# Kernel optimization log

Hardware: AMD Instinct MI355X
Metric: run time of the kernel (lower is better)

The kernel has to match this reference:

```python
import jax, jax.numpy as jnp
import numpy as np
import math

B_ = 32      # input capsule types
C_ = 32      # output capsule types
K = 3        # kernel
STRIDE = 2
H = 4
HH = H * H
ITER = 3
EPS = 1e-10
LN_2PI = math.log(2.0 * math.pi)


def setup_inputs() -> dict:
    key = jax.random.key(0)
    k1, k2, k3, k4, k5 = jax.random.split(key, 5)
    b, win = 8, 14
    poses = jax.random.normal(k1, (b, B_, win, win, HH), jnp.float32)
    activations = jax.random.uniform(k2, (b, B_, win, win), jnp.float32)
    W = jax.random.normal(k3, (B_, K, K, C_, H, H), jnp.float32)
    beta_v = jax.random.normal(k4, (1, C_, 1, 1), jnp.float32)
    beta_a = jax.random.normal(k5, (1, C_, 1), jnp.float32)
    lambda_ = jnp.float32(0.01)
    return {"poses": poses, "activations": activations, "W": W,
            "beta_v": beta_v, "beta_a": beta_a, "lambda_": lambda_}


def _extract_patches(x, w):
    r = STRIDE * jnp.arange(w)[:, None] + jnp.arange(K)  # [w, K]
    x = x[:, :, r]
    x = x[:, :, :, :, r]        # index width   -> [b,B,w_i,Kr,w_j,Kc,...]
    return x


def _em_routing(lambda_, a_, V, beta_v, beta_a):
    # a_: [b,Bkk,Cww], V: [b,Bkk,Cww,hh]
    b, Bkk, Cww, hh = V.shape
    R = jnp.full((b, Bkk, Cww), 1.0 / C_, V.dtype)
    a = None
    mu = None
    for i in range(ITER):
        Rw = (R * a_)[..., None]                      # [b,Bkk,Cww,1]
        sum_R = Rw.sum(1)                             # [b,Cww,1]
        mu = ((Rw * V).sum(1) / sum_R)[:, None]       # [b,1,Cww,hh]
        V_minus_mu_sqr = (V - mu) ** 2                # [b,Bkk,Cww,hh]
        sigma_sq = ((Rw * V_minus_mu_sqr).sum(1) / sum_R)[:, None]  # [b,1,Cww,hh]
        log_sigma = jnp.log(jnp.sqrt(sigma_sq) + EPS)
        cost = (beta_v + log_sigma.reshape(b, C_, -1, hh)) * sum_R.reshape(b, C_, -1, 1)
        a = jax.nn.sigmoid(lambda_ * (beta_a - cost.sum(-1)))
        a = a.reshape(b, Cww)
        if i != ITER - 1:
            ln_p = -V_minus_mu_sqr / (2.0 * sigma_sq) - log_sigma - 0.5 * LN_2PI
            p = jnp.exp(ln_p)
            ap = a[:, None, :] * p.sum(-1)            # [b,Bkk,Cww]
            R = jax.lax.stop_gradient(ap / (ap.sum(2, keepdims=True) + EPS) + EPS)
    return a, mu


def reference(poses, activations, W, beta_v, beta_a, lambda_):
    b = poses.shape[0]
    win = poses.shape[2]
    w = (win - K) // STRIDE + 1
    Bkk = K * K * B_
    Cww = w * w * C_

    # pose patches, ordered exactly like torch: stacked over (j outer, i inner)
    pp = _extract_patches(poses, w)                 # [b,B,w_i,Kr,w_j,Kc,hh]
    pp = pp.transpose(0, 1, 3, 5, 4, 2, 6)          # [b,B,Kr,Kc,w_j,w_i,hh]
    pp = pp.reshape(b, B_, K, K, w, w, H, H)

    # votes: W[B,Kr,Kc,C,p,q] @ pose[...,q,r]
    votes = jnp.einsum('Buvcpq,bBuvxyqr->bBuvcxypr', W, pp)
    votes = votes.reshape(b, Bkk, Cww, HH)

    # activation patches, repeated over C to match Cww=(C,w,w) flatten order
    ap = _extract_patches(activations, w)           # [b,B,w_i,Kr,w_j,Kc]
    ap = ap.transpose(0, 1, 3, 5, 4, 2).reshape(b, Bkk, w * w)
    a_ = jnp.broadcast_to(ap[:, :, None, :], (b, Bkk, C_, w * w)).reshape(b, Bkk, Cww)

    a, mu = _em_routing(lambda_, a_, votes, beta_v, beta_a)
    return mu.reshape(b, C_, w, w, HH), a.reshape(b, C_, w, w)
```

## Files before the change

### kernel.cpp

```cpp
#include <hip/hip_runtime.h>
#include <math.h>

#define NB   8
#define BC   32
#define WIN  14
#define HH   16
#define BKK  288
#define CWW  1152
#define NXY  36
#define EPSF 1e-10f
#define LOG2E 1.4426950408889634f
#define LN2   0.6931471805599453f
#define L2SQ2PI 1.3257480647361593f

__device__ __forceinline__ float ex2(float x) { return __builtin_amdgcn_exp2f(x); }
__device__ __forceinline__ float lg2(float x) { return __builtin_amdgcn_logf(x); }
__device__ __forceinline__ float rcpf(float x) { return __builtin_amdgcn_rcpf(x); }

__device__ __forceinline__ float red16(float v) {
    v += __shfl_xor(v, 1);
    v += __shfl_xor(v, 2);
    v += __shfl_xor(v, 4);
    v += __shfl_xor(v, 8);
    return v;
}

__device__ __forceinline__ float4 f4mul(float s, float4 b) {
    return make_float4(s * b.x, s * b.y, s * b.z, s * b.w);
}
__device__ __forceinline__ float4 f4fma(float s, float4 b, float4 c) {
    return make_float4(fmaf(s, b.x, c.x), fmaf(s, b.y, c.y),
                       fmaf(s, b.z, c.z), fmaf(s, b.w, c.w));
}

__global__ __launch_bounds__(256)
void wt_kernel(const float4* __restrict__ W4, float4* __restrict__ Wt4) {
    int o = blockIdx.x * 256 + threadIdx.x;
    if (o < BKK * 128) {
        int c = o & 31, p = (o >> 5) & 3, m = o >> 7;
        Wt4[o] = W4[(m * 32 + c) * 4 + p];
    }
}

__global__ __launch_bounds__(256)
void rowred_kernel(const float* __restrict__ rows_part, float* __restrict__ invRowG) {
    int i = blockIdx.x * 256 + threadIdx.x;
    if (i < NB * BKK) {
        int b = i / BKK, m = i % BKK;
        float s = EPSF;
        #pragma unroll 8
        for (int j = 0; j < 72; ++j) s += rows_part[(b * 72 + j) * BKK + m];
        invRowG[i] = 1.0f / s;
    }
}

template<int STAGE, bool FINAL>
__global__ __launch_bounds__(256)
void stats_kernel(const float* __restrict__ poses,
                  const float* __restrict__ act,
                  const float4* __restrict__ Wt4,
                  const float* __restrict__ beta_v,
                  const float* __restrict__ beta_a,
                  const float* __restrict__ lam,
                  const float* __restrict__ aws_in,
                  const float* __restrict__ psum,
                  const float* __restrict__ invRowG,
                  float* __restrict__ mu_out,
                  float* __restrict__ K2n_out,
                  float* __restrict__ C2n_out,
                  float* __restrict__ a_out)
{
    __shared__ float4 poseS4[BKK * 4];
    __shared__ float2 AE[BKK];
    __shared__ float4 red4[4 * 16 * 9];

    const int bid   = blockIdx.x;
    const int chalf = bid & 1;
    const int xy    = (bid >> 1) % NXY;
    const int b     = bid / 72;
    const int X = xy / 6, Y = xy % 6;

    const int tid = threadIdx.x;
    const int c_l = tid & 15;
    const int mch = tid >> 4;
    const int c   = chalf * 16 + c_l;
    const int n   = c * NXY + xy;

    const float4* poses4 = reinterpret_cast<const float4*>(poses);
    for (int idx = tid; idx < BKK * 4; idx += 256) {
        int m = idx >> 2, q = idx & 3;
        int B = m / 9, uv = m % 9, u = uv / 3, v = uv % 3;
        poseS4[idx] = poses4[((b * BC + B) * 196 + (2 * Y + u) * WIN + (2 * X + v)) * 4 + q];
    }
    for (int m = tid; m < BKK; m += 256) {
        int B = m / 9, uv = m % 9, u = uv / 3, v = uv % 3;
        float am = act[(b * BC + B) * 196 + (2 * Y + u) * WIN + (2 * X + v)];
        float ai, ea;
        if constexpr (STAGE == 0) { ai = am * (1.0f / 32.0f); ea = 0.0f; }
        else { ai = am * invRowG[b * BKK + m]; ea = EPSF * am; }
        AE[m] = make_float2(ai, ea);
    }

    float ap_n = 0.0f;
    const float* psum_b = nullptr;
    if constexpr (STAGE >= 1) {
        ap_n   = aws_in[(b * NXY + xy) * 32 + c];
        psum_b = psum + ((b * BKK) * NXY + xy) * 32 + c;
    }
    __syncthreads();

    const float4* WtB = Wt4 + c;

    float  sum_R = 0.0f;
    float4 sRV[4]  = {make_float4(0,0,0,0), make_float4(0,0,0,0), make_float4(0,0,0,0), make_float4(0,0,0,0)};
    float4 sRV2[4] = {make_float4(0,0,0,0), make_float4(0,0,0,0), make_float4(0,0,0,0), make_float4(0,0,0,0)};

    const int m0 = mch * 18;
    #pragma unroll 3
    for (int i = 0; i < 18; ++i) {
        int m = m0 + i;
        float4 w0 = WtB[m * 128 +  0];
        float4 w1 = WtB[m * 128 + 32];
        float4 w2 = WtB[m * 128 + 64];
        float4 w3 = WtB[m * 128 + 96];
        float4 P0 = poseS4[m * 4 + 0];
        float4 P1 = poseS4[m * 4 + 1];
        float4 P2 = poseS4[m * 4 + 2];
        float4 P3 = poseS4[m * 4 + 3];
        float4 V0 = f4fma(w0.w, P3, f4fma(w0.z, P2, f4fma(w0.y, P1, f4mul(w0.x, P0))));
        float4 V1 = f4fma(w1.w, P3, f4fma(w1.z, P2, f4fma(w1.y, P1, f4mul(w1.x, P0))));
        float4 V2 = f4fma(w2.w, P3, f4fma(w2.z, P2, f4fma(w2.y, P1, f4mul(w2.x, P0))));
        float4 V3 = f4fma(w3.w, P3, f4fma(w3.z, P2, f4fma(w3.y, P1, f4mul(w3.x, P0))));
        float Ra;
        if constexpr (STAGE == 0) {
            Ra = AE[m].x;
        } else {
            float ps = psum_b[m * (NXY * 32)];
            float2 ae = AE[m];
            Ra = fmaf(ap_n * ps, ae.x, ae.y);
        }
        sum_R += Ra;
        sRV[0] = f4fma(Ra, V0, sRV[0]);
        sRV[1] = f4fma(Ra, V1, sRV[1]);
        sRV[2] = f4fma(Ra, V2, sRV[2]);
        sRV[3] = f4fma(Ra, V3, sRV[3]);
        float4 q0 = make_float4(V0.x*V0.x, V0.y*V0.y, V0.z*V0.z, V0.w*V0.w);
        float4 q1 = make_float4(V1.x*V1.x, V1.y*V1.y, V1.z*V1.z, V1.w*V1.w);
        float4 q2 = make_float4(V2.x*V2.x, V2.y*V2.y, V2.z*V2.z, V2.w*V2.w);
        float4 q3 = make_float4(V3.x*V3.x, V3.y*V3.y, V3.z*V3.z, V3.w*V3.w);
        sRV2[0] = f4fma(Ra, q0, sRV2[0]);
        sRV2[1] = f4fma(Ra, q1, sRV2[1]);
        sRV2[2] = f4fma(Ra, q2, sRV2[2]);
        sRV2[3] = f4fma(Ra, q3, sRV2[3]);
    }

    {
        float* f1 = reinterpret_cast<float*>(sRV);
        float* f2 = reinterpret_cast<float*>(sRV2);
        #pragma unroll
        for (int k = 0; k < 16; ++k) { f1[k] += __shfl_xor(f1[k], 16); f2[k] += __shfl_xor(f2[k], 16); }
        sum_R += __shfl_xor(sum_R, 16);
        #pragma unroll
        for (int k = 0; k < 16; ++k) { f1[k] += __shfl_xor(f1[k], 32); f2[k] += __shfl_xor(f2[k], 32); }
        sum_R += __shfl_xor(sum_R, 32);
    }
    const int wgrp = tid >> 6;
    if ((tid & 48) == 0) {
        float4* dst = &red4[(wgrp * 16 + c_l) * 9];
        dst[0] = make_float4(sum_R, 0.f, 0.f, 0.f);
        dst[1] = sRV[0];  dst[2] = sRV[1];  dst[3] = sRV[2];  dst[4] = sRV[3];
        dst[5] = sRV2[0]; dst[6] = sRV2[1]; dst[7] = sRV2[2]; dst[8] = sRV2[3];
    }
    __syncthreads();

    const int h  = tid & 15;
    const int cc = tid >> 4;
    const float* red = reinterpret_cast<const float*>(red4);
    float sR = 0.f, sV = 0.f, sV2 = 0.f;
    #pragma unroll
    for (int j = 0; j < 4; ++j) {
        int off = (j * 16 + cc) * 36;
        sR  += red[off];
        sV  += red[off + 4 + h];
        sV2 += red[off + 20 + h];
    }
    float inv = 1.0f / sR;
    float mu  = sV * inv;
    float sig = fmaxf(fmaf(-mu, mu, sV2 * inv), 1e-30f);
    float l2s = lg2(sqrtf(sig) + EPSF);
    float lsum = red16(l2s) * LN2;
    int   cg   = chalf * 16 + cc;
    float cost = sR * fmaf(16.0f, beta_v[cg], lsum);
    float z    = lam[0] * (beta_a[cg] - cost);
    float av   = rcpf(1.0f + ex2(-z * LOG2E));

    int nn   = cg * NXY + xy;
    int base = (b * CWW + nn) * HH + h;
    mu_out[base] = mu;
    if constexpr (!FINAL) {
        K2n_out[base] = (-0.5f * LOG2E) / sig;
        C2n_out[base] = -(l2s + L2SQ2PI);
        if (h == 0) a_out[(b * NXY + xy) * 32 + cg] = av;
    } else {
        if (h == 0) a_out[b * CWW + nn] = av;
    }
}

__global__ __launch_bounds__(256)
void pv_kernel(const float* __restrict__ poses,
               const float4* __restrict__ Wt4,
               const float4* __restrict__ mu4,
               const float4* __restrict__ K4,
               const float4* __restrict__ C4,
               const float* __restrict__ aws,
               float* __restrict__ psum_out,
               float* __restrict__ rows_part)
{
    __shared__ float4 poseS4[BKK * 4];

    const int bid   = blockIdx.x;
    const int chalf = bid & 1;
    const int xy    = (bid >> 1) % NXY;
    const int b     = bid / 72;
    const int X = xy / 6, Y = xy % 6;

    const int tid = threadIdx.x;
    const int c_l = tid & 15;
    const int mch = tid >> 4;
    const int c   = chalf * 16 + c_l;
    const int n   = c * NXY + xy;

    const float4* poses4 = reinterpret_cast<const float4*>(poses);
    for (int idx = tid; idx < BKK * 4; idx += 256) {
        int m = idx >> 2, q = idx & 3;
        int B = m / 9, uv = m % 9, u = uv / 3, v = uv % 3;
        poseS4[idx] = poses4[((b * BC + B) * 196 + (2 * Y + u) * WIN + (2 * X + v)) * 4 + q];
    }

    float4 M[4], Kk[4], Cc[4];
    {
        int nb4 = (b * CWW + n) * 4;
        #pragma unroll
        for (int p = 0; p < 4; ++p) { M[p] = mu4[nb4 + p]; Kk[p] = K4[nb4 + p]; Cc[p] = C4[nb4 + p]; }
    }
    const float ap = aws[(b * NXY + xy) * 32 + c];
    __syncthreads();

    const float4* WtB = Wt4 + c;
    float* ps_out = psum_out + ((b * BKK) * NXY + xy) * 32 + c;
    const int rbase = bid * BKK;

    const int m0 = mch * 18;
    #pragma unroll 3
    for (int i = 0; i < 18; ++i) {
        int m = m0 + i;
        float4 w0 = WtB[m * 128 +  0];
        float4 w1 = WtB[m * 128 + 32];
        float4 w2 = WtB[m * 128 + 64];
        float4 w3 = WtB[m * 128 + 96];
        float4 P0 = poseS4[m * 4 + 0];
        float4 P1 = poseS4[m * 4 + 1];
        float4 P2 = poseS4[m * 4 + 2];
        float4 P3 = poseS4[m * 4 + 3];
        float4 V0 = f4fma(w0.w, P3, f4fma(w0.z, P2, f4fma(w0.y, P1, f4mul(w0.x, P0))));
        float4 V1 = f4fma(w1.w, P3, f4fma(w1.z, P2, f4fma(w1.y, P1, f4mul(w1.x, P0))));
        float4 V2 = f4fma(w2.w, P3, f4fma(w2.z, P2, f4fma(w2.y, P1, f4mul(w2.x, P0))));
        float4 V3 = f4fma(w3.w, P3, f4fma(w3.z, P2, f4fma(w3.y, P1, f4mul(w3.x, P0))));

        float psv = 0.0f;
        {
            float4 t, g;
            t = make_float4(V0.x-M[0].x, V0.y-M[0].y, V0.z-M[0].z, V0.w-M[0].w);
            g = make_float4(fmaf(t.x*t.x, Kk[0].x, Cc[0].x), fmaf(t.y*t.y, Kk[0].y, Cc[0].y),
                            fmaf(t.z*t.z, Kk[0].z, Cc[0].z), fmaf(t.w*t.w, Kk[0].w, Cc[0].w));
            psv += ex2(g.x) + ex2(g.y) + ex2(g.z) + ex2(g.w);
            t = make_float4(V1.x-M[1].x, V1.y-M[1].y, V1.z-M[1].z, V1.w-M[1].w);
            g = make_float4(fmaf(t.x*t.x, Kk[1].x, Cc[1].x), fmaf(t.y*t.y, Kk[1].y, Cc[1].y),
                            fmaf(t.z*t.z, Kk[1].z, Cc[1].z), fmaf(t.w*t.w, Kk[1].w, Cc[1].w));
            psv += ex2(g.x) + ex2(g.y) + ex2(g.z) + ex2(g.w);
            t = make_float4(V2.x-M[2].x, V2.y-M[2].y, V2.z-M[2].z, V2.w-M[2].w);
            g = make_float4(fmaf(t.x*t.x, Kk[2].x, Cc[2].x), fmaf(t.y*t.y, Kk[2].y, Cc[2].y),
                            fmaf(t.z*t.z, Kk[2].z, Cc[2].z), fmaf(t.w*t.w, Kk[2].w, Cc[2].w));
            psv += ex2(g.x) + ex2(g.y) + ex2(g.z) + ex2(g.w);
            t = make_float4(V3.x-M[3].x, V3.y-M[3].y, V3.z-M[3].z, V3.w-M[3].w);
            g = make_float4(fmaf(t.x*t.x, Kk[3].x, Cc[3].x), fmaf(t.y*t.y, Kk[3].y, Cc[3].y),
                            fmaf(t.z*t.z, Kk[3].z, Cc[3].z), fmaf(t.w*t.w, Kk[3].w, Cc[3].w));
            psv += ex2(g.x) + ex2(g.y) + ex2(g.z) + ex2(g.w);
        }
        ps_out[m * (NXY * 32)] = psv;

        float rv = ap * psv;
        rv += __shfl_xor(rv, 1);
        rv += __shfl_xor(rv, 2);
        rv += __shfl_xor(rv, 4);
        rv += __shfl_xor(rv, 8);
        if (c_l == 0) rows_part[rbase + m] = rv;
    }
}

extern "C" void kernel_launch(void* const* d_in, const int* in_sizes, int n_in,
                              void* d_out, int out_size, void* d_ws, size_t ws_size,
                              hipStream_t stream) {
    const float* poses  = (const float*)d_in[0];
    const float* act    = (const float*)d_in[1];
    const float* W      = (const float*)d_in[2];
    const float* beta_v = (const float*)d_in[3];
    const float* beta_a = (const float*)d_in[4];
    const float* lam    = (const float*)d_in[5];
    float* out = (float*)d_out;
    float* ws  = (float*)d_ws;

    const int SZ = NB * CWW * HH;
    float* Wt   = ws;
    float* mu   = Wt + SZ;
    float* K2n  = mu + SZ;
    float* C2n  = K2n + SZ;
    float* aws  = C2n + SZ;
    float* rows = aws + NB * CWW;
    float* invR = rows + NB * 72 * BKK;
    float* psum = invR + NB * BKK;

    const float4* Wt4 = (const float4*)Wt;

    wt_kernel<<<dim3(144), dim3(256), 0, stream>>>((const float4*)W, (float4*)Wt);

    stats_kernel<0, false><<<dim3(576), dim3(256), 0, stream>>>(
        poses, act, Wt4, beta_v, beta_a, lam, nullptr, nullptr, nullptr,
        mu, K2n, C2n, aws);
    pv_kernel<<<dim3(576), dim3(256), 0, stream>>>(
        poses, Wt4, (const float4*)mu, (const float4*)K2n, (const float4*)C2n,
        aws, psum, rows);
    rowred_kernel<<<dim3(9), dim3(256), 0, stream>>>(rows, invR);
    stats_kernel<1, false><<<dim3(576), dim3(256), 0, stream>>>(
        poses, act, Wt4, beta_v, beta_a, lam, aws, psum, invR,
        mu, K2n, C2n, aws);
    pv_kernel<<<dim3(576), dim3(256), 0, stream>>>(
        poses, Wt4, (const float4*)mu, (const float4*)K2n, (const float4*)C2n,
        aws, psum, rows);
    rowred_kernel<<<dim3(9), dim3(256), 0, stream>>>(rows, invR);
    stats_kernel<1, true><<<dim3(576), dim3(256), 0, stream>>>(
        poses, act, Wt4, beta_v, beta_a, lam, aws, psum, invR,
        out, nullptr, nullptr, out + SZ);
}
```

Measured before the change: 180.2 us.

## Fuse routing iterations into one persistent kernel with grid barriers

Replaces the chain of stats, pv and row-reduction kernels with a single persistent kernel of 576 blocks. Each block keeps its pose patch, per-row probabilities, mu/K/C and activations in shared memory across iterations, so those intermediates no longer go through global memory. Grid-wide atomic barriers stand in for the kernel boundaries at the row-sum dependency. This removes several launches and most global traffic, but it depends on all 576 blocks being co-resident (launch bounds request 3 per CU) and adds spin-wait barrier cost.

```diff
diff --git a/kernel.cpp b/kernel.cpp
--- a/kernel.cpp
+++ b/kernel.cpp
@@ -8,6 +8,7 @@
 #define BKK  288
 #define CWW  1152
 #define NXY  36
+#define NBLK 576
 #define EPSF 1e-10f
 #define LOG2E 1.4426950408889634f
 #define LN2   0.6931471805599453f
@@ -42,74 +43,27 @@
     }
 }
 
-__global__ __launch_bounds__(256)
-void rowred_kernel(const float* __restrict__ rows_part, float* __restrict__ invRowG) {
-    int i = blockIdx.x * 256 + threadIdx.x;
-    if (i < NB * BKK) {
-        int b = i / BKK, m = i % BKK;
-        float s = EPSF;
-        #pragma unroll 8
-        for (int j = 0; j < 72; ++j) s += rows_part[(b * 72 + j) * BKK + m];
-        invRowG[i] = 1.0f / s;
-    }
+__device__ __forceinline__ void gridbar(unsigned* bar, unsigned target) {
+    __syncthreads();
+    if (threadIdx.x == 0) {
+        __threadfence();
+        atomicAdd(bar, 1u);
+        while (atomicAdd(bar, 0u) < target) __builtin_amdgcn_s_sleep(2);
+        __threadfence();
+    }
+    __syncthreads();
 }
 
 template<int STAGE, bool FINAL>
-__global__ __launch_bounds__(256)
-void stats_kernel(const float* __restrict__ poses,
-                  const float* __restrict__ act,
-                  const float4* __restrict__ Wt4,
-                  const float* __restrict__ beta_v,
-                  const float* __restrict__ beta_a,
-                  const float* __restrict__ lam,
-                  const float* __restrict__ aws_in,
-                  const float* __restrict__ psum,
-                  const float* __restrict__ invRowG,
-                  float* __restrict__ mu_out,
-                  float* __restrict__ K2n_out,
-                  float* __restrict__ C2n_out,
-                  float* __restrict__ a_out)
+__device__ __forceinline__ void stats_phase(
+    const float4* __restrict__ WtB, const float4* poseS4, const float* psumS,
+    const float* actS, const float* AIS, float* red, float* mKC, float* aS,
+    const float* __restrict__ beta_v, const float* __restrict__ beta_a,
+    float lamv, int tid, int c_l, int mch, int chalf, int xy, int b,
+    float* __restrict__ out)
 {
-    __shared__ float4 poseS4[BKK * 4];
-    __shared__ float2 AE[BKK];
-    __shared__ float4 red4[4 * 16 * 9];
-
-    const int bid   = blockIdx.x;
-    const int chalf = bid & 1;
-    const int xy    = (bid >> 1) % NXY;
-    const int b     = bid / 72;
-    const int X = xy / 6, Y = xy % 6;
-
-    const int tid = threadIdx.x;
-    const int c_l = tid & 15;
-    const int mch = tid >> 4;
-    const int c   = chalf * 16 + c_l;
-    const int n   = c * NXY + xy;
-
-    const float4* poses4 = reinterpret_cast<const float4*>(poses);
-    for (int idx = tid; idx < BKK * 4; idx += 256) {
-        int m = idx >> 2, q = idx & 3;
-        int B = m / 9, uv = m % 9, u = uv / 3, v = uv % 3;
-        poseS4[idx] = poses4[((b * BC + B) * 196 + (2 * Y + u) * WIN + (2 * X + v)) * 4 + q];
-    }
-    for (int m = tid; m < BKK; m += 256) {
-        int B = m / 9, uv = m % 9, u = uv / 3, v = uv % 3;
-        float am = act[(b * BC + B) * 196 + (2 * Y + u) * WIN + (2 * X + v)];
-        float ai, ea;
-        if constexpr (STAGE == 0) { ai = am * (1.0f / 32.0f); ea = 0.0f; }
-        else { ai = am * invRowG[b * BKK + m]; ea = EPSF * am; }
-        AE[m] = make_float2(ai, ea);
-    }
-
     float ap_n = 0.0f;
-    const float* psum_b = nullptr;
-    if constexpr (STAGE >= 1) {
-        ap_n   = aws_in[(b * NXY + xy) * 32 + c];
-        psum_b = psum + ((b * BKK) * NXY + xy) * 32 + c;
-    }
-    __syncthreads();
-
-    const float4* WtB = Wt4 + c;
+    if constexpr (STAGE >= 1) ap_n = aS[c_l];
 
     float  sum_R = 0.0f;
     float4 sRV[4]  = {make_float4(0,0,0,0), make_float4(0,0,0,0), make_float4(0,0,0,0), make_float4(0,0,0,0)};
@@ -118,7 +72,7 @@
     const int m0 = mch * 18;
     #pragma unroll 3
     for (int i = 0; i < 18; ++i) {
-        int m = m0 + i;
+        const int m = m0 + i;
         float4 w0 = WtB[m * 128 +  0];
         float4 w1 = WtB[m * 128 + 32];
         float4 w2 = WtB[m * 128 + 64];
@@ -133,56 +87,50 @@
         float4 V3 = f4fma(w3.w, P3, f4fma(w3.z, P2, f4fma(w3.y, P1, f4mul(w3.x, P0))));
         float Ra;
         if constexpr (STAGE == 0) {
-            Ra = AE[m].x;
+            Ra = AIS[m];
         } else {
-            float ps = psum_b[m * (NXY * 32)];
-            float2 ae = AE[m];
-            Ra = fmaf(ap_n * ps, ae.x, ae.y);
+            float ps = psumS[m * 17 + c_l];
+            Ra = fmaf(ap_n * ps, AIS[m], EPSF * actS[m]);
         }
         sum_R += Ra;
         sRV[0] = f4fma(Ra, V0, sRV[0]);
         sRV[1] = f4fma(Ra, V1, sRV[1]);
         sRV[2] = f4fma(Ra, V2, sRV[2]);
         sRV[3] = f4fma(Ra, V3, sRV[3]);
-        float4 q0 = make_float4(V0.x*V0.x, V0.y*V0.y, V0.z*V0.z, V0.w*V0.w);
-        float4 q1 = make_float4(V1.x*V1.x, V1.y*V1.y, V1.z*V1.z, V1.w*V1.w);
-        float4 q2 = make_float4(V2.x*V2.x, V2.y*V2.y, V2.z*V2.z, V2.w*V2.w);
-        float4 q3 = make_float4(V3.x*V3.x, V3.y*V3.y, V3.z*V3.z, V3.w*V3.w);
-        sRV2[0] = f4fma(Ra, q0, sRV2[0]);
-        sRV2[1] = f4fma(Ra, q1, sRV2[1]);
-        sRV2[2] = f4fma(Ra, q2, sRV2[2]);
-        sRV2[3] = f4fma(Ra, q3, sRV2[3]);
-    }
-
-    {
-        float* f1 = reinterpret_cast<float*>(sRV);
-        float* f2 = reinterpret_cast<float*>(sRV2);
+        sRV2[0] = f4fma(Ra, make_float4(V0.x*V0.x, V0.y*V0.y, V0.z*V0.z, V0.w*V0.w), sRV2[0]);
+        sRV2[1] = f4fma(Ra, make_float4(V1.x*V1.x, V1.y*V1.y, V1.z*V1.z, V1.w*V1.w), sRV2[1]);
+        sRV2[2] = f4fma(Ra, make_float4(V2.x*V2.x, V2.y*V2.y, V2.z*V2.z, V2.w*V2.w), sRV2[2]);
+        sRV2[3] = f4fma(Ra, make_float4(V3.x*V3.x, V3.y*V3.y, V3.z*V3.z, V3.w*V3.w), sRV2[3]);
+    }
+
+    float* f1 = reinterpret_cast<float*>(sRV);
+    float* f2 = reinterpret_cast<float*>(sRV2);
+    #pragma unroll
+    for (int k = 0; k < 16; ++k) { f1[k] += __shfl_xor(f1[k], 16); f2[k] += __shfl_xor(f2[k], 16); }
+    sum_R += __shfl_xor(sum_R, 16);
+    #pragma unroll
+    for (int k = 0; k < 16; ++k) { f1[k] += __shfl_xor(f1[k], 32); f2[k] += __shfl_xor(f2[k], 32); }
+    sum_R += __shfl_xor(sum_R, 32);
+
+    __syncthreads();
+    if ((tid & 48) == 0) {
+        int wv = tid >> 6;
+        float* dst = red + (wv * 16 + c_l) * 33;
+        dst[0] = sum_R;
         #pragma unroll
-        for (int k = 0; k < 16; ++k) { f1[k] += __shfl_xor(f1[k], 16); f2[k] += __shfl_xor(f2[k], 16); }
-        sum_R += __shfl_xor(sum_R, 16);
-        #pragma unroll
-        for (int k = 0; k < 16; ++k) { f1[k] += __shfl_xor(f1[k], 32); f2[k] += __shfl_xor(f2[k], 32); }
-        sum_R += __shfl_xor(sum_R, 32);
-    }
-    const int wgrp = tid >> 6;
-    if ((tid & 48) == 0) {
-        float4* dst = &red4[(wgrp * 16 + c_l) * 9];
-        dst[0] = make_float4(sum_R, 0.f, 0.f, 0.f);
-        dst[1] = sRV[0];  dst[2] = sRV[1];  dst[3] = sRV[2];  dst[4] = sRV[3];
-        dst[5] = sRV2[0]; dst[6] = sRV2[1]; dst[7] = sRV2[2]; dst[8] = sRV2[3];
+        for (int k = 0; k < 16; ++k) { dst[1 + k] = f1[k]; dst[17 + k] = f2[k]; }
     }
     __syncthreads();
 
     const int h  = tid & 15;
     const int cc = tid >> 4;
-    const float* red = reinterpret_cast<const float*>(red4);
     float sR = 0.f, sV = 0.f, sV2 = 0.f;
     #pragma unroll
     for (int j = 0; j < 4; ++j) {
-        int off = (j * 16 + cc) * 36;
-        sR  += red[off];
-        sV  += red[off + 4 + h];
-        sV2 += red[off + 20 + h];
+        const float* rr = red + (j * 16 + cc) * 33;
+        sR  += rr[0];
+        sV  += rr[1 + h];
+        sV2 += rr[17 + h];
     }
     float inv = 1.0f / sR;
     float mu  = sV * inv;
@@ -191,69 +139,40 @@
     float lsum = red16(l2s) * LN2;
     int   cg   = chalf * 16 + cc;
     float cost = sR * fmaf(16.0f, beta_v[cg], lsum);
-    float z    = lam[0] * (beta_a[cg] - cost);
+    float z    = lamv * (beta_a[cg] - cost);
     float av   = rcpf(1.0f + ex2(-z * LOG2E));
 
-    int nn   = cg * NXY + xy;
-    int base = (b * CWW + nn) * HH + h;
-    mu_out[base] = mu;
     if constexpr (!FINAL) {
-        K2n_out[base] = (-0.5f * LOG2E) / sig;
-        C2n_out[base] = -(l2s + L2SQ2PI);
-        if (h == 0) a_out[(b * NXY + xy) * 32 + cg] = av;
+        mKC[0 * 256 + h * 16 + cc] = mu;
+        mKC[1 * 256 + h * 16 + cc] = (-0.5f * LOG2E) / sig;
+        mKC[2 * 256 + h * 16 + cc] = -(l2s + L2SQ2PI);
+        if (h == 0) aS[cc] = av;
     } else {
-        if (h == 0) a_out[b * CWW + nn] = av;
-    }
-}
-
-__global__ __launch_bounds__(256)
-void pv_kernel(const float* __restrict__ poses,
-               const float4* __restrict__ Wt4,
-               const float4* __restrict__ mu4,
-               const float4* __restrict__ K4,
-               const float4* __restrict__ C4,
-               const float* __restrict__ aws,
-               float* __restrict__ psum_out,
-               float* __restrict__ rows_part)
+        int nn = cg * NXY + xy;
+        out[(b * CWW + nn) * HH + h] = mu;
+        if (h == 0) out[NB * CWW * HH + b * CWW + nn] = av;
+    }
+    __syncthreads();
+}
+
+__device__ __forceinline__ void pv_phase(
+    const float4* __restrict__ WtB, const float4* poseS4, float* psumS,
+    const float* mKC, const float* aS, float* __restrict__ rows,
+    int bid, int c_l, int mch)
 {
-    __shared__ float4 poseS4[BKK * 4];
-
-    const int bid   = blockIdx.x;
-    const int chalf = bid & 1;
-    const int xy    = (bid >> 1) % NXY;
-    const int b     = bid / 72;
-    const int X = xy / 6, Y = xy % 6;
-
-    const int tid = threadIdx.x;
-    const int c_l = tid & 15;
-    const int mch = tid >> 4;
-    const int c   = chalf * 16 + c_l;
-    const int n   = c * NXY + xy;
-
-    const float4* poses4 = reinterpret_cast<const float4*>(poses);
-    for (int idx = tid; idx < BKK * 4; idx += 256) {
-        int m = idx >> 2, q = idx & 3;
-        int B = m / 9, uv = m % 9, u = uv / 3, v = uv % 3;
-        poseS4[idx] = poses4[((b * BC + B) * 196 + (2 * Y + u) * WIN + (2 * X + v)) * 4 + q];
-    }
-
-    float4 M[4], Kk[4], Cc[4];
-    {
-        int nb4 = (b * CWW + n) * 4;
-        #pragma unroll
-        for (int p = 0; p < 4; ++p) { M[p] = mu4[nb4 + p]; Kk[p] = K4[nb4 + p]; Cc[p] = C4[nb4 + p]; }
-    }
-    const float ap = aws[(b * NXY + xy) * 32 + c];
-    __syncthreads();
-
-    const float4* WtB = Wt4 + c;
-    float* ps_out = psum_out + ((b * BKK) * NXY + xy) * 32 + c;
-    const int rbase = bid * BKK;
+    float M[16], Kk[16], Cc[16];
+    #pragma unroll
+    for (int h2 = 0; h2 < 16; ++h2) {
+        M[h2]  = mKC[          h2 * 16 + c_l];
+        Kk[h2] = mKC[256 +     h2 * 16 + c_l];
+        Cc[h2] = mKC[512 +     h2 * 16 + c_l];
+    }
+    const float ap = aS[c_l];
 
     const int m0 = mch * 18;
-    #pragma unroll 3
+    #pragma unroll 2
     for (int i = 0; i < 18; ++i) {
-        int m = m0 + i;
+        const int m = m0 + i;
         float4 w0 = WtB[m * 128 +  0];
         float4 w1 = WtB[m * 128 + 32];
         float4 w2 = WtB[m * 128 + 64];
@@ -268,34 +187,107 @@
         float4 V3 = f4fma(w3.w, P3, f4fma(w3.z, P2, f4fma(w3.y, P1, f4mul(w3.x, P0))));
 
         float psv = 0.0f;
-        {
-            float4 t, g;
-            t = make_float4(V0.x-M[0].x, V0.y-M[0].y, V0.z-M[0].z, V0.w-M[0].w);
-            g = make_float4(fmaf(t.x*t.x, Kk[0].x, Cc[0].x), fmaf(t.y*t.y, Kk[0].y, Cc[0].y),
-                            fmaf(t.z*t.z, Kk[0].z, Cc[0].z), fmaf(t.w*t.w, Kk[0].w, Cc[0].w));
-            psv += ex2(g.x) + ex2(g.y) + ex2(g.z) + ex2(g.w);
-            t = make_float4(V1.x-M[1].x, V1.y-M[1].y, V1.z-M[1].z, V1.w-M[1].w);
-            g = make_float4(fmaf(t.x*t.x, Kk[1].x, Cc[1].x), fmaf(t.y*t.y, Kk[1].y, Cc[1].y),
-                            fmaf(t.z*t.z, Kk[1].z, Cc[1].z), fmaf(t.w*t.w, Kk[1].w, Cc[1].w));
-            psv += ex2(g.x) + ex2(g.y) + ex2(g.z) + ex2(g.w);
-            t = make_float4(V2.x-M[2].x, V2.y-M[2].y, V2.z-M[2].z, V2.w-M[2].w);
-            g = make_float4(fmaf(t.x*t.x, Kk[2].x, Cc[2].x), fmaf(t.y*t.y, Kk[2].y, Cc[2].y),
-                            fmaf(t.z*t.z, Kk[2].z, Cc[2].z), fmaf(t.w*t.w, Kk[2].w, Cc[2].w));
-            psv += ex2(g.x) + ex2(g.y) + ex2(g.z) + ex2(g.w);
-            t = make_float4(V3.x-M[3].x, V3.y-M[3].y, V3.z-M[3].z, V3.w-M[3].w);
-            g = make_float4(fmaf(t.x*t.x, Kk[3].x, Cc[3].x), fmaf(t.y*t.y, Kk[3].y, Cc[3].y),
-                            fmaf(t.z*t.z, Kk[3].z, Cc[3].z), fmaf(t.w*t.w, Kk[3].w, Cc[3].w));
-            psv += ex2(g.x) + ex2(g.y) + ex2(g.z) + ex2(g.w);
-        }
-        ps_out[m * (NXY * 32)] = psv;
+        float t;
+        t = V0.x - M[0];  psv += ex2(fmaf(t * t, Kk[0],  Cc[0]));
+        t = V0.y - M[1];  psv += ex2(fmaf(t * t, Kk[1],  Cc[1]));
+        t = V0.z - M[2];  psv += ex2(fmaf(t * t, Kk[2],  Cc[2]));
+        t = V0.w - M[3];  psv += ex2(fmaf(t * t, Kk[3],  Cc[3]));
+        t = V1.x - M[4];  psv += ex2(fmaf(t * t, Kk[4],  Cc[4]));
+        t = V1.y - M[5];  psv += ex2(fmaf(t * t, Kk[5],  Cc[5]));
+        t = V1.z - M[6];  psv += ex2(fmaf(t * t, Kk[6],  Cc[6]));
+        t = V1.w - M[7];  psv += ex2(fmaf(t * t, Kk[7],  Cc[7]));
+        t = V2.x - M[8];  psv += ex2(fmaf(t * t, Kk[8],  Cc[8]));
+        t = V2.y - M[9];  psv += ex2(fmaf(t * t, Kk[9],  Cc[9]));
+        t = V2.z - M[10]; psv += ex2(fmaf(t * t, Kk[10], Cc[10]));
+        t = V2.w - M[11]; psv += ex2(fmaf(t * t, Kk[11], Cc[11]));
+        t = V3.x - M[12]; psv += ex2(fmaf(t * t, Kk[12], Cc[12]));
+        t = V3.y - M[13]; psv += ex2(fmaf(t * t, Kk[13], Cc[13]));
+        t = V3.z - M[14]; psv += ex2(fmaf(t * t, Kk[14], Cc[14]));
+        t = V3.w - M[15]; psv += ex2(fmaf(t * t, Kk[15], Cc[15]));
+
+        psumS[m * 17 + c_l] = psv;
 
         float rv = ap * psv;
         rv += __shfl_xor(rv, 1);
         rv += __shfl_xor(rv, 2);
         rv += __shfl_xor(rv, 4);
         rv += __shfl_xor(rv, 8);
-        if (c_l == 0) rows_part[rbase + m] = rv;
-    }
+        if (c_l == 0) rows[bid * BKK + m] = rv;
+    }
+}
+
+__device__ __forceinline__ void rowred_phase(
+    const float* __restrict__ rows, const float* actS, float* AIS, int b, int tid)
+{
+    for (int m = tid; m < BKK; m += 256) {
+        float s = EPSF;
+        const float* rp = rows + b * 72 * BKK + m;
+        #pragma unroll 8
+        for (int j = 0; j < 72; ++j) s += rp[j * BKK];
+        AIS[m] = actS[m] / s;
+    }
+    __syncthreads();
+}
+
+__global__ __launch_bounds__(256, 3)
+void fused_kernel(const float* __restrict__ poses,
+                  const float* __restrict__ act,
+                  const float4* __restrict__ Wt4,
+                  const float* __restrict__ beta_v,
+                  const float* __restrict__ beta_a,
+                  const float* __restrict__ lam,
+                  float* __restrict__ rows0,
+                  float* __restrict__ rows1,
+                  unsigned* __restrict__ bar,
+                  float* __restrict__ out)
+{
+    __shared__ float4 poseS4[BKK * 4];
+    __shared__ float  psumS[BKK * 17];
+    __shared__ float  actS[BKK];
+    __shared__ float  AIS[BKK];
+    __shared__ float  mKC[3 * 256];
+    __shared__ float  aS[16];
+
+    const int bid   = blockIdx.x;
+    const int chalf = bid & 1;
+    const int xy    = (bid >> 1) % NXY;
+    const int b     = bid / 72;
+    const int X = xy / 6, Y = xy % 6;
+
+    const int tid = threadIdx.x;
+    const int c_l = tid & 15;
+    const int mch = tid >> 4;
+    const int c   = chalf * 16 + c_l;
+
+    const float4* poses4 = reinterpret_cast<const float4*>(poses);
+    for (int idx = tid; idx < BKK * 4; idx += 256) {
+        int m = idx >> 2, q = idx & 3;
+        int B = m / 9, uv = m % 9, u = uv / 3, v = uv % 3;
+        poseS4[idx] = poses4[((b * BC + B) * 196 + (2 * Y + u) * WIN + (2 * X + v)) * 4 + q];
+    }
+    for (int m = tid; m < BKK; m += 256) {
+        int B = m / 9, uv = m % 9, u = uv / 3, v = uv % 3;
+        float am = act[(b * BC + B) * 196 + (2 * Y + u) * WIN + (2 * X + v)];
+        actS[m] = am;
+        AIS[m]  = am * (1.0f / 32.0f);
+    }
+    __syncthreads();
+
+    const float4* WtB = Wt4 + c;
+    const float lamv = lam[0];
+
+    stats_phase<0, false>(WtB, poseS4, psumS, actS, AIS, psumS, mKC, aS,
+                          beta_v, beta_a, lamv, tid, c_l, mch, chalf, xy, b, out);
+    pv_phase(WtB, poseS4, psumS, mKC, aS, rows0, bid, c_l, mch);
+    gridbar(bar, NBLK);
+    rowred_phase(rows0, actS, AIS, b, tid);
+    stats_phase<1, false>(WtB, poseS4, psumS, actS, AIS, psumS, mKC, aS,
+                          beta_v, beta_a, lamv, tid, c_l, mch, chalf, xy, b, out);
+    pv_phase(WtB, poseS4, psumS, mKC, aS, rows1, bid, c_l, mch);
+    gridbar(bar, 2 * NBLK);
+    rowred_phase(rows1, actS, AIS, b, tid);
+    stats_phase<1, true>(WtB, poseS4, psumS, actS, AIS, psumS, mKC, aS,
+                         beta_v, beta_a, lamv, tid, c_l, mch, chalf, xy, b, out);
 }
 
 extern "C" void kernel_launch(void* const* d_in, const int* in_sizes, int n_in,
@@ -310,35 +302,14 @@
     float* out = (float*)d_out;
     float* ws  = (float*)d_ws;
 
-    const int SZ = NB * CWW * HH;
-    float* Wt   = ws;
-    float* mu   = Wt + SZ;
-    float* K2n  = mu + SZ;
-    float* C2n  = K2n + SZ;
-    float* aws  = C2n + SZ;
-    float* rows = aws + NB * CWW;
-    float* invR = rows + NB * 72 * BKK;
-    float* psum = invR + NB * BKK;
-
-    const float4* Wt4 = (const float4*)Wt;
-
+    unsigned* bar = (unsigned*)ws;
+    float* Wt    = ws + 16;
+    float* rows0 = Wt + BKK * 128 * 4;
+    float* rows1 = rows0 + NBLK * BKK;
+
+    hipMemsetAsync((void*)bar, 0, 64, stream);
     wt_kernel<<<dim3(144), dim3(256), 0, stream>>>((const float4*)W, (float4*)Wt);
-
-    stats_kernel<0, false><<<dim3(576), dim3(256), 0, stream>>>(
-        poses, act, Wt4, beta_v, beta_a, lam, nullptr, nullptr, nullptr,
-        mu, K2n, C2n, aws);
-    pv_kernel<<<dim3(576), dim3(256), 0, stream>>>(
-        poses, Wt4, (const float4*)mu, (const float4*)K2n, (const float4*)C2n,
-        aws, psum, rows);
-    rowred_kernel<<<dim3(9), dim3(256), 0, stream>>>(rows, invR);
-    stats_kernel<1, false><<<dim3(576), dim3(256), 0, stream>>>(
-        poses, act, Wt4, beta_v, beta_a, lam, aws, psum, invR,
-        mu, K2n, C2n, aws);
-    pv_kernel<<<dim3(576), dim3(256), 0, stream>>>(
-        poses, Wt4, (const float4*)mu, (const float4*)K2n, (const float4*)C2n,
-        aws, psum, rows);
-    rowred_kernel<<<dim3(9), dim3(256), 0, stream>>>(rows, invR);
-    stats_kernel<1, true><<<dim3(576), dim3(256), 0, stream>>>(
-        poses, act, Wt4, beta_v, beta_a, lam, aws, psum, invR,
-        out, nullptr, nullptr, out + SZ);
-}
+    fused_kernel<<<dim3(NBLK), dim3(256), 0, stream>>>(
+        poses, act, (const float4*)Wt, beta_v, beta_a, lam,
+        rows0, rows1, bar, out);
+}
```

Result: slower. 313.1 us (+73.7%).
